# Performance work log

Measured on AMD Instinct MI355X. Metric: run time of the kernel, lower is better.

Reference implementation:

```python
import jax, jax.numpy as jnp
import numpy as np

B, S = 1, 1536
D_MODEL, NHEAD, HEAD_DIM = 1024, 16, 64
ROPE, NUM_SEQ = 32, 4
KVC, QC, D_FF = 256, 384, 4096
SPP = S // NUM_SEQ                      # seq per stock = 384
EPS_RMS = 1.1920929e-07                 # torch RMSNorm default eps = finfo(fp32).eps
ATTN_EPS = 1e-5
LAMBDA_INIT = 0.8 - 0.6 * float(np.exp(-0.3 * 0.0))  # depth 0 -> 0.2
SCALING = float(((HEAD_DIM + ROPE) // 2) ** -0.5)


def rmsnorm(x, w, eps=EPS_RMS):
    var = jnp.mean(jnp.square(x), axis=-1, keepdims=True)
    return x * jax.lax.rsqrt(var + eps) * w


def setup_inputs() -> dict:
    key = jax.random.key(0)
    ks = jax.random.split(key, 16)
    sd = 0.02
    inv_freq = 1.0 / (10000.0 ** (np.arange(0, ROPE // 4) / (ROPE // 4)))
    ang = np.arange(1, SPP)[:, None] * inv_freq[None, :]  # [SPP-1, ROPE//4]
    return {
        "x": jax.random.normal(ks[0], (B, S, D_MODEL), jnp.float32),
        "freqs_cos": jnp.asarray(np.cos(ang), jnp.float32),
        "freqs_sin": jnp.asarray(np.sin(ang), jnp.float32),
        "norm1_w": jnp.ones((D_MODEL,), jnp.float32),
        "norm2_w": jnp.ones((D_MODEL,), jnp.float32),
        "kv_down_w": jax.random.normal(ks[1], (KVC + ROPE, D_MODEL), jnp.float32) * sd,
        "q_down_w": jax.random.normal(ks[2], (QC, D_MODEL), jnp.float32) * sd,
        "kv_norm_w": jnp.ones((KVC,), jnp.float32),
        "q_norm_w": jnp.ones((QC,), jnp.float32),
        "kv_up_w": jax.random.normal(ks[3], (HEAD_DIM * NHEAD * 2, KVC), jnp.float32) * sd,
        "q_up_w": jax.random.normal(ks[4], ((HEAD_DIM + ROPE) * NHEAD, QC), jnp.float32) * sd,
        "lambda_q1": jax.random.normal(ks[5], (HEAD_DIM // 2,), jnp.float32) * 0.1,
        "lambda_k1": jax.random.normal(ks[6], (HEAD_DIM // 2,), jnp.float32) * 0.1,
        "lambda_q2": jax.random.normal(ks[7], (HEAD_DIM // 2,), jnp.float32) * 0.1,
        "lambda_k2": jax.random.normal(ks[8], (HEAD_DIM // 2,), jnp.float32) * 0.1,
        "attn_norm_w": jnp.ones((HEAD_DIM,), jnp.float32),
        "o_w": jax.random.normal(ks[9], (D_MODEL, NHEAD * HEAD_DIM), jnp.float32) * sd,
        "ff_in_w": jax.random.normal(ks[10], (D_FF * 2, D_MODEL), jnp.float32) * sd,
        "ff_out_w": jax.random.normal(ks[11], (D_MODEL, D_FF), jnp.float32) * sd,
    }


def reference(x, freqs_cos, freqs_sin, norm1_w, norm2_w, kv_down_w, q_down_w,
              kv_norm_w, q_norm_w, kv_up_w, q_up_w, lambda_q1, lambda_k1,
              lambda_q2, lambda_k2, attn_norm_w, o_w, ff_in_w, ff_out_w):
    b, s, _ = x.shape
    spp = s // NUM_SEQ
    H2, hd2 = 2 * NHEAD, HEAD_DIM // 2

    # block-tiled causal mask (1 = masked), matching mask.repeat(..., num_seq, num_seq)
    base = jnp.triu(jnp.ones((spp, spp), jnp.float32), 1)
    mask = jnp.tile(base, (NUM_SEQ, NUM_SEQ))  # [S, S]

    xin = rmsnorm(x, norm1_w)
    ckv = xin @ kv_down_w.T                                    # [B,S,KVC+ROPE]
    c_kv, k_rope = ckv[..., :KVC], ckv[..., KVC:]
    kv = (rmsnorm(c_kv, kv_norm_w) @ kv_up_w.T).reshape(b, s, NHEAD, 2 * HEAD_DIM)
    k, v = kv[..., :HEAD_DIM], kv[..., HEAD_DIM:]
    k = k.reshape(b, s, H2, hd2)
    qf = (rmsnorm(xin @ q_down_w.T, q_norm_w) @ q_up_w.T).reshape(b, s, NHEAD, HEAD_DIM + ROPE)
    q, q_rope = qf[..., :HEAD_DIM], qf[..., HEAD_DIM:]
    q = q.reshape(b, s, H2, hd2)
    k_rope = jnp.tile(k_rope[:, :, None, :], (1, 1, NHEAD, 1)).reshape(b, s, H2, ROPE // 2)
    q_rope = q_rope.reshape(b, s, H2, ROPE // 2)

    # rotary emb; position 0 of every ticker is left untouched (identity rotation)
    cos = jnp.concatenate([jnp.ones((1, ROPE // 4), freqs_cos.dtype), freqs_cos], 0)  # [spp, ROPE//4]
    sin = jnp.concatenate([jnp.zeros((1, ROPE // 4), freqs_sin.dtype), freqs_sin], 0)

    def rot(r):
        # S is laid out as (position, ticker) interleaved: s = p*NUM_SEQ + t
        r = r.reshape(b, spp, NUM_SEQ, H2, ROPE // 4, 2)
        c = cos[None, :, None, None, :]
        s_ = sin[None, :, None, None, :]
        r0, r1 = r[..., 0], r[..., 1]
        y = jnp.stack([r0 * c - r1 * s_, r0 * s_ + r1 * c], axis=-1)
        return y.reshape(b, s, H2, ROPE // 2)

    q = jnp.concatenate([q, rot(q_rope)], -1).transpose(0, 2, 1, 3)  # [B,2H,S,dk]
    k = jnp.concatenate([k, rot(k_rope)], -1).transpose(0, 2, 1, 3)
    v = v.transpose(0, 2, 1, 3)                                      # [B,H,S,hd]

    a = jnp.einsum('bhqd,bhkd->bhqk', q, k) * SCALING
    a = jnp.where(mask[None, None] == 1, -1e9, a)
    a = jax.nn.softmax(a, axis=-1)

    lam = jnp.exp(jnp.sum(lambda_k1 * lambda_q1)) - jnp.exp(jnp.sum(lambda_k2 * lambda_q2)) + LAMBDA_INIT
    a = a.reshape(b, NHEAD, 2, s, s)
    a1, a2 = a[:, :, 0], a[:, :, 1]
    g = jnp.mean(a1, axis=-2, keepdims=True)            # [B,H,1,S], broadcasts over queries
    a = a1 - lam * a2 + lam * g
    a = jnp.where(mask[None, None] == 1, 0.0, a)

    out = jnp.einsum('bhqk,bhkd->bhqd', a, v)           # [B,H,S,hd]
    out = rmsnorm(out.transpose(0, 2, 1, 3), attn_norm_w, eps=ATTN_EPS).transpose(0, 2, 1, 3)
    # faithful to source: raw reshape of [B,H,S,hd] -> [B,S,H*hd] (transposes cancel)
    out = out.reshape(b, s, NHEAD * HEAD_DIM)
    x = x + out @ o_w.T

    h = rmsnorm(x, norm2_w)
    uv = h @ ff_in_w.T
    u, vg = uv[..., :D_FF], uv[..., D_FF:]
    return x + (u * jax.nn.silu(vg)) @ ff_out_w.T
```

## Files before the change

### kernel.cpp

```cpp
#include <hip/hip_runtime.h>
#include <math.h>

#define S     1536
#define DM    1024
#define NH    16
#define H2N   32
#define HD    64
#define KVC   256
#define QC    384
#define DFF   4096
#define SPP   384
#define DQK   48
#define CKW   672
#define EPS_RMS  1.1920929e-07f
#define ATTN_EPS 1e-5f
#define SCALING  0.14433756729740643f

typedef float f32x4 __attribute__((ext_vector_type(4)));
typedef float f32x16 __attribute__((ext_vector_type(16)));
typedef short bf16x8 __attribute__((ext_vector_type(8)));

__device__ __forceinline__ short cvt_bf16(float f) {
  union { float f; unsigned u; } x; x.f = f;
  unsigned r = x.u + 0x7FFFu + ((x.u >> 16) & 1u);
  return (short)(r >> 16);
}
__device__ __forceinline__ unsigned pk2(float a, float b) {
  unsigned r;
  asm("v_cvt_pk_bf16_f32 %0, %1, %2" : "=v"(r) : "v"(a), "v"(b));
  return r;
}
__device__ __forceinline__ bf16x8 cvt8(float4 a, float4 b) {
  union { unsigned u[4]; bf16x8 v; } r;
  r.u[0] = pk2(a.x, a.y); r.u[1] = pk2(a.z, a.w);
  r.u[2] = pk2(b.x, b.y); r.u[3] = pk2(b.z, b.w);
  return r.v;
}
__device__ __forceinline__ int swz8(int flat, int nwg) {
  if (nwg & 7) return flat;
  return (flat & 7) * (nwg >> 3) + (flat >> 3);
}

__global__ __launch_bounds__(256) void cvt_w4(const float* __restrict__ s0, int n0,
    const float* __restrict__ s1, int n1, const float* __restrict__ s2, int n2,
    const float* __restrict__ s3, int n3, short* __restrict__ dst) {
  long base = (long)blockIdx.x * 2048 + (long)threadIdx.x * 8;
  const float* src; long off;
  if (base < n0) { src = s0; off = base; }
  else if (base < (long)n0 + n1) { src = s1; off = base - n0; }
  else if (base < (long)n0 + n1 + n2) { src = s2; off = base - n0 - n1; }
  else { src = s3; off = base - n0 - n1 - n2; }
  float4 a = *reinterpret_cast<const float4*>(src + off);
  float4 b = *reinterpret_cast<const float4*>(src + off + 4);
  *reinterpret_cast<bf16x8*>(dst + base) = cvt8(a, b);
}

__global__ __launch_bounds__(256) void rmsnorm_bf(const float* __restrict__ in,
    const float* __restrict__ w, short* __restrict__ out,
    int cols, int ldin, int ldout, float eps) {
  const int row = blockIdx.x;
  const float* xr = in + (size_t)row * ldin;
  short* yr = out + (size_t)row * ldout;
  const int tid = threadIdx.x;
  float ss = 0.f;
  for (int c = tid << 2; c < cols; c += 1024) {
    float4 v = *reinterpret_cast<const float4*>(xr + c);
    ss += v.x*v.x + v.y*v.y + v.z*v.z + v.w*v.w;
  }
#pragma unroll
  for (int mm = 1; mm < 64; mm <<= 1) ss += __shfl_xor(ss, mm, 64);
  __shared__ float red[4];
  if ((tid & 63) == 0) red[tid >> 6] = ss;
  __syncthreads();
  float tot = red[0] + red[1] + red[2] + red[3];
  float scale = rsqrtf(tot / (float)cols + eps);
  for (int c = tid << 2; c < cols; c += 1024) {
    float4 v = *reinterpret_cast<const float4*>(xr + c);
    float4 wv = *reinterpret_cast<const float4*>(w + c);
    uint2 p;
    p.x = pk2(v.x*scale*wv.x, v.y*scale*wv.y);
    p.y = pk2(v.z*scale*wv.z, v.w*scale*wv.w);
    *reinterpret_cast<uint2*>(yr + c) = p;
  }
}

__global__ __launch_bounds__(256) void rmsnorm2_bf(const float* __restrict__ comb,
    const float* __restrict__ w0, const float* __restrict__ w1,
    short* __restrict__ o0, short* __restrict__ o1, float eps) {
  const int row = blockIdx.x;
  const int seg = blockIdx.y;
  const float* xr = comb + (size_t)row * CKW + (seg ? 288 : 0);
  const float* w  = seg ? w1 : w0;
  short* yr = seg ? (o1 + (size_t)row * QC) : (o0 + (size_t)row * KVC);
  const int cols = seg ? QC : KVC;
  const int tid = threadIdx.x;
  float ss = 0.f;
  for (int c = tid << 2; c < cols; c += 1024) {
    float4 v = *reinterpret_cast<const float4*>(xr + c);
    ss += v.x*v.x + v.y*v.y + v.z*v.z + v.w*v.w;
  }
#pragma unroll
  for (int mm = 1; mm < 64; mm <<= 1) ss += __shfl_xor(ss, mm, 64);
  __shared__ float red[4];
  if ((tid & 63) == 0) red[tid >> 6] = ss;
  __syncthreads();
  float tot = red[0] + red[1] + red[2] + red[3];
  float scale = rsqrtf(tot / (float)cols + eps);
  for (int c = tid << 2; c < cols; c += 1024) {
    float4 v = *reinterpret_cast<const float4*>(xr + c);
    float4 wv = *reinterpret_cast<const float4*>(w + c);
    uint2 p;
    p.x = pk2(v.x*scale*wv.x, v.y*scale*wv.y);
    p.y = pk2(v.z*scale*wv.z, v.w*scale*wv.w);
    *reinterpret_cast<uint2*>(yr + c) = p;
  }
}

__global__ __launch_bounds__(256) void rmsnorm_sum_bf(const float* __restrict__ p0,
    const float* __restrict__ p1, const float* __restrict__ xres,
    const float* __restrict__ w, float* __restrict__ outw, short* __restrict__ yb,
    float eps) {
  const int row = blockIdx.x;
  const int c = threadIdx.x << 2;
  const size_t base = (size_t)row * DM + c;
  float4 a = *reinterpret_cast<const float4*>(p0 + base);
  float4 b = *reinterpret_cast<const float4*>(p1 + base);
  float4 xv = *reinterpret_cast<const float4*>(xres + base);
  float4 v = make_float4(a.x+b.x+xv.x, a.y+b.y+xv.y, a.z+b.z+xv.z, a.w+b.w+xv.w);
  *reinterpret_cast<float4*>(outw + base) = v;
  float ss = v.x*v.x + v.y*v.y + v.z*v.z + v.w*v.w;
#pragma unroll
  for (int mm = 1; mm < 64; mm <<= 1) ss += __shfl_xor(ss, mm, 64);
  __shared__ float red[4];
  if ((threadIdx.x & 63) == 0) red[threadIdx.x >> 6] = ss;
  __syncthreads();
  float tot = red[0] + red[1] + red[2] + red[3];
  float scale = rsqrtf(tot * (1.0f / (float)DM) + eps);
  float4 wv = *reinterpret_cast<const float4*>(w + c);
  uint2 p;
  p.x = pk2(v.x*scale*wv.x, v.y*scale*wv.y);
  p.y = pk2(v.z*scale*wv.z, v.w*scale*wv.w);
  *reinterpret_cast<uint2*>(yb + base) = p;
}

__global__ __launch_bounds__(256) void fadd2(float* __restrict__ out,
    const float* __restrict__ p0, const float* __restrict__ p1) {
  size_t i = ((size_t)blockIdx.x * 256 + threadIdx.x) << 2;
  float4 o = *reinterpret_cast<float4*>(out + i);
  float4 a = *reinterpret_cast<const float4*>(p0 + i);
  float4 b = *reinterpret_cast<const float4*>(p1 + i);
  o.x += a.x + b.x; o.y += a.y + b.y; o.z += a.z + b.z; o.w += a.w + b.w;
  *reinterpret_cast<float4*>(out + i) = o;
}

template<int ADD>
__global__ __launch_bounds__(256) void mgemm_nt(const short* __restrict__ A,
    const short* __restrict__ B, const float* __restrict__ src, float* __restrict__ C,
    int M, int N, int K, int lda, int ldb, int ldc) {
  __shared__ short As[64][72];
  __shared__ short Bs[64][72];
  const int nwg = gridDim.x * gridDim.y;
  const int sfl = swz8(blockIdx.y * gridDim.x + blockIdx.x, nwg);
  const int bxs = sfl % gridDim.x, bys = sfl / gridDim.x;
  const int bm = bys * 64, bn = bxs * 64;
  const int tid = threadIdx.x;
  const int w = tid >> 6, lane = tid & 63;
  const int wr = (w >> 1) << 5, wc = (w & 1) << 5;
  const int srow = tid >> 2, sk = (tid & 3) << 4;
  const int lrow = lane & 15, lk8 = (lane >> 4) << 3;
  const int arow = bm + srow, brow = bn + srow;
  const bool bvalid = brow < N;
  f32x4 acc[2][2];
#pragma unroll
  for (int i = 0; i < 2; ++i)
#pragma unroll
    for (int j = 0; j < 2; ++j) acc[i][j] = (f32x4){0.f, 0.f, 0.f, 0.f};

  bf16x8 rah0, rah1, rbh0, rbh1;
  {
    const short* ap = A + (size_t)arow * lda + sk;
    rah0 = *reinterpret_cast<const bf16x8*>(ap);
    rah1 = *reinterpret_cast<const bf16x8*>(ap + 8);
  }
  rbh0 = (bf16x8){0,0,0,0,0,0,0,0}; rbh1 = rbh0;
  if (bvalid) {
    const short* bp = B + (size_t)brow * ldb + sk;
    rbh0 = *reinterpret_cast<const bf16x8*>(bp);
    rbh1 = *reinterpret_cast<const bf16x8*>(bp + 8);
  }

  for (int k0 = 0; k0 < K; k0 += 64) {
    bf16x8 va0 = rah0, va1 = rah1, vb0 = rbh0, vb1 = rbh1;
    __syncthreads();
    *reinterpret_cast<bf16x8*>(&As[srow][sk])     = va0;
    *reinterpret_cast<bf16x8*>(&As[srow][sk + 8]) = va1;
    *reinterpret_cast<bf16x8*>(&Bs[srow][sk])     = vb0;
    *reinterpret_cast<bf16x8*>(&Bs[srow][sk + 8]) = vb1;
    __syncthreads();
// ... 41 lines not shown

__global__ __launch_bounds__(256) void mgemm_dual(const short* __restrict__ A0,
    const short* __restrict__ B0, float* __restrict__ C0,
    const short* __restrict__ A1, const short* __restrict__ B1, float* __restrict__ C1) {
  __shared__ short As[64][72];
  __shared__ short Bs[64][72];
  const int flat = blockIdx.x;
  const short *A, *B; float* C;
  int K, lda, ldb, ldc, bm, bn;
  if (flat < 768) {
    const int sfl = swz8(flat, 768);
    bm = (sfl / 32) * 64; bn = (sfl % 32) * 64;
    A = A0; B = B0; C = C0; K = KVC; lda = KVC; ldb = KVC; ldc = 2048;
  } else {
    const int sfl = swz8(flat - 768, 576);
    bm = (sfl / 24) * 64; bn = (sfl % 24) * 64;
    A = A1; B = B1; C = C1; K = QC; lda = QC; ldb = QC; ldc = 1536;
  }
  const int tid = threadIdx.x;
  const int w = tid >> 6, lane = tid & 63;
  const int wr = (w >> 1) << 5, wc = (w & 1) << 5;
  const int srow = tid >> 2, sk = (tid & 3) << 4;
  const int lrow = lane & 15, lk8 = (lane >> 4) << 3;
  const int arow = bm + srow, brow = bn + srow;
  f32x4 acc[2][2];
#pragma unroll
  for (int i = 0; i < 2; ++i)
#pragma unroll
    for (int j = 0; j < 2; ++j) acc[i][j] = (f32x4){0.f, 0.f, 0.f, 0.f};

  bf16x8 rah0, rah1, rbh0, rbh1;
  {
    const short* ap = A + (size_t)arow * lda + sk;
    rah0 = *reinterpret_cast<const bf16x8*>(ap);
    rah1 = *reinterpret_cast<const bf16x8*>(ap + 8);
    const short* bp = B + (size_t)brow * ldb + sk;
    rbh0 = *reinterpret_cast<const bf16x8*>(bp);
    rbh1 = *reinterpret_cast<const bf16x8*>(bp + 8);
  }
  for (int k0 = 0; k0 < K; k0 += 64) {
    bf16x8 va0 = rah0, va1 = rah1, vb0 = rbh0, vb1 = rbh1;
    __syncthreads();
    *reinterpret_cast<bf16x8*>(&As[srow][sk])     = va0;
    *reinterpret_cast<bf16x8*>(&As[srow][sk + 8]) = va1;
    *reinterpret_cast<bf16x8*>(&Bs[srow][sk])     = vb0;
    *reinterpret_cast<bf16x8*>(&Bs[srow][sk + 8]) = vb1;
    __syncthreads();
    const int kn = k0 + 64;
    if (kn < K) {
      const short* ap = A + (size_t)arow * lda + kn + sk;
      rah0 = *reinterpret_cast<const bf16x8*>(ap);
      rah1 = *reinterpret_cast<const bf16x8*>(ap + 8);
      const short* bp = B + (size_t)brow * ldb + kn + sk;
      rbh0 = *reinterpret_cast<const bf16x8*>(bp);
      rbh1 = *reinterpret_cast<const bf16x8*>(bp + 8);
    }
#pragma unroll
    for (int kk = 0; kk < 2; ++kk) {
      bf16x8 af0 = *reinterpret_cast<bf16x8*>(&As[wr + lrow][(kk << 5) + lk8]);
      bf16x8 af1 = *reinterpret_cast<bf16x8*>(&As[wr + 16 + lrow][(kk << 5) + lk8]);
      bf16x8 bf0 = *reinterpret_cast<bf16x8*>(&Bs[wc + lrow][(kk << 5) + lk8]);
      bf16x8 bf1 = *reinterpret_cast<bf16x8*>(&Bs[wc + 16 + lrow][(kk << 5) + lk8]);
      acc[0][0] = __builtin_amdgcn_mfma_f32_16x16x32_bf16(af0, bf0, acc[0][0], 0, 0, 0);
      acc[0][1] = __builtin_amdgcn_mfma_f32_16x16x32_bf16(af0, bf1, acc[0][1], 0, 0, 0);
      acc[1][0] = __builtin_amdgcn_mfma_f32_16x16x32_bf16(af1, bf0, acc[1][0], 0, 0, 0);
      acc[1][1] = __builtin_amdgcn_mfma_f32_16x16x32_bf16(af1, bf1, acc[1][1], 0, 0, 0);
    }
  }
  const int crow0 = bm + wr + ((lane >> 4) << 2);
  const int ccol0 = bn + wc + lrow;
#pragma unroll
  for (int mi = 0; mi < 2; ++mi)
#pragma unroll
    for (int ni = 0; ni < 2; ++ni) {
      int colc = ccol0 + (ni << 4);
#pragma unroll
      for (int r = 0; r < 4; ++r) {
        int rowc = crow0 + (mi << 4) + r;
        C[(size_t)rowc * ldc + colc] = acc[mi][ni][r];
      }
    }
}

__global__ __launch_bounds__(256) void mgemm_sk(const short* __restrict__ A,
    const short* __restrict__ B, float* __restrict__ P0, float* __restrict__ P1,
    int M, int N, int K2, int lda, int ldb, int ldc) {
  __shared__ short As[64][72];
  __shared__ short Bs[64][72];
  const int nwg = gridDim.x * gridDim.y;
  const int sfl = swz8(blockIdx.y * gridDim.x + blockIdx.x, nwg);
  const int bxs = sfl % gridDim.x, bys = sfl / gridDim.x;
  const int bm = bys * 64, bn = bxs * 64;
  const int koff = blockIdx.z * K2;
  float* C = blockIdx.z ? P1 : P0;
  const int tid = threadIdx.x;
  const int w = tid >> 6, lane = tid & 63;
  const int wr = (w >> 1) << 5, wc = (w & 1) << 5;
  const int srow = tid >> 2, sk = (tid & 3) << 4;
  const int lrow = lane & 15, lk8 = (lane >> 4) << 3;
  const int arow = bm + srow, brow = bn + srow;
  f32x4 acc[2][2];
#pragma unroll
  for (int i = 0; i < 2; ++i)
#pragma unroll
    for (int j = 0; j < 2; ++j) acc[i][j] = (f32x4){0.f, 0.f, 0.f, 0.f};

  bf16x8 rah0, rah1, rbh0, rbh1;
  {
    const short* ap = A + (size_t)arow * lda + koff + sk;
    rah0 = *reinterpret_cast<const bf16x8*>(ap);
    rah1 = *reinterpret_cast<const bf16x8*>(ap + 8);
    const short* bp = B + (size_t)brow * ldb + koff + sk;
    rbh0 = *reinterpret_cast<const bf16x8*>(bp);
    rbh1 = *reinterpret_cast<const bf16x8*>(bp + 8);
  }
  const int kend = koff + K2;
  for (int k0 = koff; k0 < kend; k0 += 64) {
    bf16x8 va0 = rah0, va1 = rah1, vb0 = rbh0, vb1 = rbh1;
    __syncthreads();
    *reinterpret_cast<bf16x8*>(&As[srow][sk])     = va0;
    *reinterpret_cast<bf16x8*>(&As[srow][sk + 8]) = va1;
    *reinterpret_cast<bf16x8*>(&Bs[srow][sk])     = vb0;
    *reinterpret_cast<bf16x8*>(&Bs[srow][sk + 8]) = vb1;
    __syncthreads();
    const int kn = k0 + 64;
    if (kn < kend) {
      const short* ap = A + (size_t)arow * lda + kn + sk;
      rah0 = *reinterpret_cast<const bf16x8*>(ap);
      rah1 = *reinterpret_cast<const bf16x8*>(ap + 8);
      const short* bp = B + (size_t)brow * ldb + kn + sk;
      rbh0 = *reinterpret_cast<const bf16x8*>(bp);
      rbh1 = *reinterpret_cast<const bf16x8*>(bp + 8);
    }
#pragma unroll
    for (int kk = 0; kk < 2; ++kk) {
      bf16x8 af0 = *reinterpret_cast<bf16x8*>(&As[wr + lrow][(kk << 5) + lk8]);
      bf16x8 af1 = *reinterpret_cast<bf16x8*>(&As[wr + 16 + lrow][(kk << 5) + lk8]);
      bf16x8 bf0 = *reinterpret_cast<bf16x8*>(&Bs[wc + lrow][(kk << 5) + lk8]);
      bf16x8 bf1 = *reinterpret_cast<bf16x8*>(&Bs[wc + 16 + lrow][(kk << 5) + lk8]);
      acc[0][0] = __builtin_amdgcn_mfma_f32_16x16x32_bf16(af0, bf0, acc[0][0], 0, 0, 0);
      acc[0][1] = __builtin_amdgcn_mfma_f32_16x16x32_bf16(af0, bf1, acc[0][1], 0, 0, 0);
      acc[1][0] = __builtin_amdgcn_mfma_f32_16x16x32_bf16(af1, bf0, acc[1][0], 0, 0, 0);
      acc[1][1] = __builtin_amdgcn_mfma_f32_16x16x32_bf16(af1, bf1, acc[1][1], 0, 0, 0);
    }
  }
  const int crow0 = bm + wr + ((lane >> 4) << 2);
  const int ccol0 = bn + wc + lrow;
#pragma unroll
  for (int mi = 0; mi < 2; ++mi)
#pragma unroll
    for (int ni = 0; ni < 2; ++ni) {
      int colc = ccol0 + (ni << 4);
#pragma unroll
      for (int r = 0; r < 4; ++r) {
        int rowc = crow0 + (mi << 4) + r;
        C[(size_t)rowc * ldc + colc] = acc[mi][ni][r];
      }
    }
}

__global__ __launch_bounds__(256) void mgemm_glu(const short* __restrict__ A,
    const short* __restrict__ Bw, short* __restrict__ C,
    int M, int N, int K, int lda, int ldb, int ldc) {
  __shared__ short As[128][72];
  __shared__ short Bu[64][72];
  __shared__ short Bv[64][72];
  const int nwg = gridDim.x * gridDim.y;
  const int sfl = swz8(blockIdx.y * gridDim.x + blockIdx.x, nwg);
  const int bxs = sfl % gridDim.x, bys = sfl / gridDim.x;
  const int bm = bys * 128, bn = bxs * 64;
  const int tid = threadIdx.x;
  const int w = tid >> 6, lane = tid & 63;
  const int wr = (w >> 1) << 6, wc = (w & 1) << 5;
  const int arow = bm + (tid >> 1), ac = (tid & 1) << 5;
  const int brow = bn + (tid >> 2), bc = (tid & 3) << 4;
  const int lrow = lane & 15, lk8 = (lane >> 4) << 3;
  f32x4 au[4][2], av[4][2];
#pragma unroll
  for (int i = 0; i < 4; ++i)
#pragma unroll
    for (int j = 0; j < 2; ++j) {
      au[i][j] = (f32x4){0.f, 0.f, 0.f, 0.f};
      av[i][j] = (f32x4){0.f, 0.f, 0.f, 0.f};
    }
  bf16x8 ra[4], ru[2], rv[2];
  {
    const short* ap = A + (size_t)arow * lda + ac;
    const short* up = Bw + (size_t)brow * ldb + bc;
    const short* vp = Bw + (size_t)(N + brow) * ldb + bc;
#pragma unroll
    for (int e = 0; e < 4; ++e) ra[e] = *reinterpret_cast<const bf16x8*>(ap + (e << 3));
    ru[0] = *reinterpret_cast<const bf16x8*>(up);
    ru[1] = *reinterpret_cast<const bf16x8*>(up + 8);
    rv[0] = *reinterpret_cast<const bf16x8*>(vp);
    rv[1] = *reinterpret_cast<const bf16x8*>(vp + 8);
  }
  for (int k0 = 0; k0 < K; k0 += 64) {
    __syncthreads();
#pragma unroll
    for (int e = 0; e < 4; ++e)
      *reinterpret_cast<bf16x8*>(&As[tid >> 1][ac + (e << 3)]) = ra[e];
    *reinterpret_cast<bf16x8*>(&Bu[tid >> 2][bc])     = ru[0];
    *reinterpret_cast<bf16x8*>(&Bu[tid >> 2][bc + 8]) = ru[1];
    *reinterpret_cast<bf16x8*>(&Bv[tid >> 2][bc])     = rv[0];
    *reinterpret_cast<bf16x8*>(&Bv[tid >> 2][bc + 8]) = rv[1];
    __syncthreads();
    const int kn = k0 + 64;
    if (kn < K) {
      const short* ap = A + (size_t)arow * lda + kn + ac;
      const short* up = Bw + (size_t)brow * ldb + kn + bc;
      const short* vp = Bw + (size_t)(N + brow) * ldb + kn + bc;
#pragma unroll
      for (int e = 0; e < 4; ++e) ra[e] = *reinterpret_cast<const bf16x8*>(ap + (e << 3));
      ru[0] = *reinterpret_cast<const bf16x8*>(up);
      ru[1] = *reinterpret_cast<const bf16x8*>(up + 8);
      rv[0] = *reinterpret_cast<const bf16x8*>(vp);
      rv[1] = *reinterpret_cast<const bf16x8*>(vp + 8);
    }
#pragma unroll
    for (int kk = 0; kk < 2; ++kk) {
      bf16x8 af[4], uf[2], vf[2];
#pragma unroll
      for (int i = 0; i < 4; ++i)
        af[i] = *reinterpret_cast<bf16x8*>(&As[wr + (i << 4) + lrow][(kk << 5) + lk8]);
#pragma unroll
      for (int j = 0; j < 2; ++j) {
        uf[j] = *reinterpret_cast<bf16x8*>(&Bu[wc + (j << 4) + lrow][(kk << 5) + lk8]);
        vf[j] = *reinterpret_cast<bf16x8*>(&Bv[wc + (j << 4) + lrow][(kk << 5) + lk8]);
      }
#pragma unroll
      for (int i = 0; i < 4; ++i)
#pragma unroll
        for (int j = 0; j < 2; ++j) {
          au[i][j] = __builtin_amdgcn_mfma_f32_16x16x32_bf16(af[i], uf[j], au[i][j], 0, 0, 0);
          av[i][j] = __builtin_amdgcn_mfma_f32_16x16x32_bf16(af[i], vf[j], av[i][j], 0, 0, 0);
        }
    }
  }
  const int crow0 = bm + wr + ((lane >> 4) << 2);
  const int ccol0 = bn + wc + lrow;
#pragma unroll
  for (int mi = 0; mi < 4; ++mi)
#pragma unroll
    for (int ni = 0; ni < 2; ++ni) {
      int colc = ccol0 + (ni << 4);
#pragma unroll
      for (int r = 0; r < 4; ++r) {
        int rowc = crow0 + (mi << 4) + r;
        float uu = au[mi][ni][r], vg = av[mi][ni][r];
        float sig = 1.0f / (1.0f + __expf(-vg));
        C[(size_t)rowc * ldc + colc] = cvt_bf16(uu * vg * sig);
      }
    }
}

__global__ __launch_bounds__(256) void prep_attn(const float* __restrict__ qf,
    const float* __restrict__ kvb, const float* __restrict__ ckv,
    const float* __restrict__ fc, const float* __restrict__ fs,
    short* __restrict__ Qb, short* __restrict__ Kb, short* __restrict__ Vt) {
  __shared__ short Ts[128][74];
  const int bx = blockIdx.x;
  if (bx < 192) {
    const int t = (bx % 6) * 256 + threadIdx.x;
    const int h2 = bx / 6;
    const int hh = h2 >> 1, par = h2 & 1;
    const float* qrow = qf + (size_t)t*1536 + hh*96;
    const float* krow = kvb + (size_t)t*2048 + hh*128;
    unsigned qu[24], ku[24];
#pragma unroll
    for (int xq = 0; xq < 8; ++xq) {
      float4 qv = *reinterpret_cast<const float4*>(qrow + par*32 + (xq<<2));
      float4 kv = *reinterpret_cast<const float4*>(krow + par*32 + (xq<<2));
      qu[xq*2]   = pk2(qv.x, qv.y); qu[xq*2+1] = pk2(qv.z, qv.w);
      ku[xq*2]   = pk2(kv.x, kv.y); ku[xq*2+1] = pk2(kv.z, kv.w);
    }
    int p = t >> 2;
    const float* qr = qrow + 64 + par*16;
    const float* kr = ckv + (size_t)t*CKW + 256 + par*16;
#pragma unroll
    for (int mq = 0; mq < 8; ++mq) {
      float c = 1.f, sn = 0.f;
      if (p > 0) { c = fc[(p-1)*8 + mq]; sn = fs[(p-1)*8 + mq]; }
      float q0 = qr[2*mq], q1 = qr[2*mq+1];
      qu[16 + mq] = pk2(q0*c - q1*sn, q0*sn + q1*c);
      float k0 = kr[2*mq], k1 = kr[2*mq+1];
      ku[16 + mq] = pk2(k0*c - k1*sn, k0*sn + k1*c);
    }
    unsigned* qo = (unsigned*)(Qb + ((size_t)h2*S + t)*DQK);
    unsigned* ko = (unsigned*)(Kb + ((size_t)h2*S + t)*DQK);
#pragma unroll
    for (int e = 0; e < 6; ++e) {
      *reinterpret_cast<uint4*>(qo + (e<<2)) = make_uint4(qu[e*4], qu[e*4+1], qu[e*4+2], qu[e*4+3]);
      *reinterpret_cast<uint4*>(ko + (e<<2)) = make_uint4(ku[e*4], ku[e*4+1], ku[e*4+2], ku[e*4+3]);
    }
  } else {
    const int f2 = bx - 192;
    const int hh = f2 % 16;
    const int t0 = (f2 / 16) << 7;
    const int tl = threadIdx.x >> 3, dp = (threadIdx.x & 7) << 3;
#pragma unroll
    for (int pass = 0; pass < 4; ++pass) {
      int t = t0 + (pass << 5) + tl;
      const float* vp = kvb + (size_t)t*2048 + hh*128 + 64 + dp;
      float4 a = *reinterpret_cast<const float4*>(vp);
      float4 b = *reinterpret_cast<const float4*>(vp + 4);
      *reinterpret_cast<bf16x8*>(&Ts[(pass << 5) + tl][dp]) = cvt8(a, b);
    }
    __syncthreads();
    for (int idx = threadIdx.x; idx < 1024; idx += 256) {
      int d = idx >> 4, tseg = (idx & 15) << 3;
      bf16x8 v;
#pragma unroll
      for (int e = 0; e < 8; ++e) v[e] = Ts[tseg + e][d];
      *reinterpret_cast<bf16x8*>(Vt + ((size_t)hh*HD + d)*S + t0 + tseg) = v;
    }
  }
}

__global__ __launch_bounds__(256) void flash_mfma(const short* __restrict__ Qb,
    const short* __restrict__ Kb, const short* __restrict__ Vg,
    float* __restrict__ Ob, float* __restrict__ rowm, float* __restrict__ rowl,
    float* __restrict__ Ob1a, float* __restrict__ Ob1b,
    float* __restrict__ rm1, float* __restrict__ rl1) {
  const int h2 = blockIdx.y;
  const int hh = h2 >> 1;
  const int z  = blockIdx.z;
  const int tid = threadIdx.x;
  const int w = tid >> 6, lane = tid & 63;
  const int ql = lane & 31, h = lane >> 5;
  const int cq = blockIdx.x / 3, k = blockIdx.x % 3;
  const int qi = k + 3*w;
  const int qbase = cq*SPP + (qi << 5);
  const int ri0w = qi << 5;

  __shared__ __align__(16) float Ot[4][32][36];

  bf16x8 qf0, qf1, qf2;
  {
    const short* qp = Qb + ((size_t)h2*S + qbase + ql)*DQK + (h << 3);
    qf0 = *reinterpret_cast<const bf16x8*>(qp);
    qf1 = *reinterpret_cast<const bf16x8*>(qp + 16);
    qf2 = *reinterpret_cast<const bf16x8*>(qp + 32);
  }
  const short* Kbase = Kb + (size_t)h2*S*DQK + (h << 3);
  const short* V0 = Vg + ((size_t)hh*HD + ql)*S + (h << 3);
  const short* V1 = Vg + ((size_t)hh*HD + 32 + ql)*S + (h << 3);

  float m = -1e30f, l = 0.f;
  f32x16 o0, o1;
#pragma unroll
  for (int r = 0; r < 16; ++r) { o0[r] = 0.f; o1[r] = 0.f; }

  for (int c = (z << 1); c < (z << 1) + 2; ++c) {
    for (int jr = 0; jr <= ri0w; jr += 32) {
      const int j0 = c*SPP + jr;
      const bool diag = (jr == ri0w);
      const short* kp = Kbase + (size_t)(j0 + ql)*DQK;
      bf16x8 kf0 = *reinterpret_cast<const bf16x8*>(kp);
      bf16x8 kf1 = *reinterpret_cast<const bf16x8*>(kp + 16);
      bf16x8 kf2 = *reinterpret_cast<const bf16x8*>(kp + 32);
      bf16x8 v00 = *reinterpret_cast<const bf16x8*>(V0 + j0);
      bf16x8 v01 = *reinterpret_cast<const bf16x8*>(V0 + j0 + 16);
      bf16x8 v10 = *reinterpret_cast<const bf16x8*>(V1 + j0);
      bf16x8 v11 = *reinterpret_cast<const bf16x8*>(V1 + j0 + 16);

      f32x16 st;
#pragma unroll
      for (int r = 0; r < 16; ++r) st[r] = 0.f;
      st = __builtin_amdgcn_mfma_f32_32x32x16_bf16(kf0, qf0, st, 0, 0, 0);
      st = __builtin_amdgcn_mfma_f32_32x32x16_bf16(kf1, qf1, st, 0, 0, 0);
      st = __builtin_amdgcn_mfma_f32_32x32x16_bf16(kf2, qf2, st, 0, 0, 0);

      if (diag) {
#pragma unroll
        for (int r = 0; r < 16; ++r) {
          int kl = (r & 3) + ((r >> 2) << 3) + (h << 2);
          st[r] = (kl <= ql) ? st[r] * SCALING : -1e30f;
        }
      } else {
#pragma unroll
        for (int r = 0; r < 16; ++r) st[r] *= SCALING;
      }

      float tm = st[0];
#pragma unroll
      for (int r = 1; r < 16; ++r) tm = fmaxf(tm, st[r]);
      tm = fmaxf(tm, __shfl_xor(tm, 32));
      if (__any(tm > m + 8.0f)) {
        float mnew = fmaxf(m, tm);
        float sc = __expf(m - mnew);
        m = mnew;
        l *= sc;
#pragma unroll
        for (int r = 0; r < 16; ++r) { o0[r] *= sc; o1[r] *= sc; }
      }
      float ps = 0.f;
#pragma unroll
      for (int r = 0; r < 16; ++r) { float p = __expf(st[r] - m); st[r] = p; ps += p; }
      ps += __shfl_xor(ps, 32);
      l += ps;

      unsigned A0 = pk2(st[0],  st[1]),  B0 = pk2(st[2],  st[3]);
      unsigned C0 = pk2(st[4],  st[5]),  D0 = pk2(st[6],  st[7]);
      unsigned A1 = pk2(st[8],  st[9]),  B1 = pk2(st[10], st[11]);
      unsigned C1 = pk2(st[12], st[13]), D1 = pk2(st[14], st[15]);
      unsigned xA0 = (unsigned)__shfl_xor((int)A0, 32), xB0 = (unsigned)__shfl_xor((int)B0, 32);
      unsigned xC0 = (unsigned)__shfl_xor((int)C0, 32), xD0 = (unsigned)__shfl_xor((int)D0, 32);
      unsigned xA1 = (unsigned)__shfl_xor((int)A1, 32), xB1 = (unsigned)__shfl_xor((int)B1, 32);
      unsigned xC1 = (unsigned)__shfl_xor((int)C1, 32), xD1 = (unsigned)__shfl_xor((int)D1, 32);
      union { unsigned u[4]; bf16x8 v; } P0, P1;
      P0.u[0] = h ? xC0 : A0;  P0.u[1] = h ? xD0 : B0;
      P0.u[2] = h ? C0 : xA0;  P0.u[3] = h ? D0 : xB0;
      P1.u[0] = h ? xC1 : A1;  P1.u[1] = h ? xD1 : B1;
      P1.u[2] = h ? C1 : xA1;  P1.u[3] = h ? D1 : xB1;

      o0 = __builtin_amdgcn_mfma_f32_32x32x16_bf16(v00, P0.v, o0, 0, 0, 0);
      o0 = __builtin_amdgcn_mfma_f32_32x32x16_bf16(v01, P1.v, o0, 0, 0, 0);
      o1 = __builtin_amdgcn_mfma_f32_32x32x16_bf16(v10, P0.v, o1, 0, 0, 0);
      o1 = __builtin_amdgcn_mfma_f32_32x32x16_bf16(v11, P1.v, o1, 0, 0, 0);
    }
  }

  float* ot = &Ot[w][0][0];
  float* orow;
  if (z == 0) orow = Ob + ((size_t)h2*S + qbase)*HD;
  else orow = (h2 < 16) ? Ob1a + ((size_t)h2*S + qbase)*HD
                        : Ob1b + ((size_t)(h2 - 16)*S + qbase)*HD;
#pragma unroll
  for (int r = 0; r < 16; ++r) {
    int dl = (r & 3) + ((r >> 2) << 3) + (h << 2);
    ot[ql*36 + dl] = o0[r];
  }
#pragma unroll
  for (int it = 0; it < 4; ++it) {
    int idx = lane + (it << 6);
    int row = idx >> 3, c4 = (idx & 7) << 2;
    float4 v = *reinterpret_cast<float4*>(&ot[row*36 + c4]);
    *reinterpret_cast<float4*>(&orow[(size_t)row*HD + c4]) = v;
  }
#pragma unroll
  for (int r = 0; r < 16; ++r) {
    int dl = (r & 3) + ((r >> 2) << 3) + (h << 2);
    ot[ql*36 + dl] = o1[r];
  }
#pragma unroll
  for (int it = 0; it < 4; ++it) {
    int idx = lane + (it << 6);
    int row = idx >> 3, c4 = (idx & 7) << 2;
    float4 v = *reinterpret_cast<float4*>(&ot[row*36 + c4]);
    *reinterpret_cast<float4*>(&orow[(size_t)row*HD + 32 + c4]) = v;
  }
  if (lane < 32) {
    if (z == 0) { rowm[h2*S + qbase + lane] = m; rowl[h2*S + qbase + lane] = l; }
    else        { rm1[h2*S + qbase + lane] = m;  rl1[h2*S + qbase + lane] = l; }
  }
}

__global__ __launch_bounds__(256) void merge_ml(float* __restrict__ rowm,
    float* __restrict__ rowl, float* __restrict__ rm1, float* __restrict__ rl1,
    const float* __restrict__ lq1, const float* __restrict__ lk1,
    const float* __restrict__ lq2, const float* __restrict__ lk2,
    float* __restrict__ lamp) {
  const int gid = blockIdx.x * 256 + threadIdx.x;
  float m0 = rowm[gid], l0 = rowl[gid], m1 = rm1[gid], l1 = rl1[gid];
  float m = fmaxf(m0, m1);
  float w0 = __expf(m0 - m), w1 = __expf(m1 - m);
  float L = l0*w0 + l1*w1;
  float linv = 1.0f / L;
  rowm[gid] = m; rowl[gid] = L;
  rm1[gid] = w0 * linv; rl1[gid] = w1 * linv;
  if (blockIdx.x == 0 && threadIdx.x < 32) {
    int t = threadIdx.x;
    float a = lq1[t]*lk1[t];
    float b = lq2[t]*lk2[t];
#pragma unroll
    for (int mm = 1; mm < 32; mm <<= 1) { a += __shfl_xor(a, mm, 32); b += __shfl_xor(b, mm, 32); }
    if (t == 0) lamp[0] = expf(a) - expf(b) + 0.2f;
  }
}

__global__ __launch_bounds__(256) void colsum_mfma(const short* __restrict__ Qb,
    const short* __restrict__ Kb, const float* __restrict__ rowm,
    const float* __restrict__ rowl, float* __restrict__ gcol) {
  const int jt = blockIdx.x;
  const int hh = blockIdx.y, h2 = hh << 1;
  const int cK = jt / 12, jr32 = jt % 12;
  const int jr = jr32 << 5;
  const int j0 = cK*SPP + jr;
  const int tid = threadIdx.x;
  const int w = tid >> 6, lane = tid & 63;
  const int ql = lane & 31, h = lane >> 5;

  bf16x8 kf0, kf1, kf2;
  {
    const short* kp = Kb + ((size_t)h2*S + j0 + ql)*DQK + (h << 3);
    kf0 = *reinterpret_cast<const bf16x8*>(kp);
    kf1 = *reinterpret_cast<const bf16x8*>(kp + 16);
    kf2 = *reinterpret_cast<const bf16x8*>(kp + 32);
  }
  const int nt = 12 - jr32;
  const int T = nt << 2;
  float gs[16];
#pragma unroll
  for (int r = 0; r < 16; ++r) gs[r] = 0.f;

  for (int tt = w; tt < T; tt += 4) {
    int cq = tt / nt, qrem = tt - cq*nt;
    int qi = jr32 + qrem;
    int i0 = cq*SPP + (qi << 5);
    const bool diag = (qrem == 0);
    const short* qp = Qb + ((size_t)h2*S + i0 + ql)*DQK + (h << 3);
    bf16x8 qf0 = *reinterpret_cast<const bf16x8*>(qp);
    bf16x8 qf1 = *reinterpret_cast<const bf16x8*>(qp + 16);
    bf16x8 qf2 = *reinterpret_cast<const bf16x8*>(qp + 32);
    f32x16 st;
#pragma unroll
    for (int r = 0; r < 16; ++r) st[r] = 0.f;
    st = __builtin_amdgcn_mfma_f32_32x32x16_bf16(kf0, qf0, st, 0, 0, 0);
    st = __builtin_amdgcn_mfma_f32_32x32x16_bf16(kf1, qf1, st, 0, 0, 0);
    st = __builtin_amdgcn_mfma_f32_32x32x16_bf16(kf2, qf2, st, 0, 0, 0);
    float Mq = rowm[h2*S + i0 + ql];
    float Lq = 1.0f / rowl[h2*S + i0 + ql];
    if (diag) {
#pragma unroll
      for (int r = 0; r < 16; ++r) {
        int kl = (r & 3) + ((r >> 2) << 3) + (h << 2);
        if (kl <= ql) gs[r] += __expf(st[r]*SCALING - Mq) * Lq;
      }
    } else {
#pragma unroll
      for (int r = 0; r < 16; ++r) gs[r] += __expf(st[r]*SCALING - Mq) * Lq;
    }
  }
  __shared__ float gw[4][32];
#pragma unroll
  for (int r = 0; r < 16; ++r) {
    float v = gs[r];
#pragma unroll
    for (int mm = 1; mm < 32; mm <<= 1) v += __shfl_xor(v, mm, 32);
    if (ql == 0) gw[w][(r & 3) + ((r >> 2) << 3) + (h << 2)] = v;
  }
  __syncthreads();
  if (tid < 32) {
    float s = gw[0][tid] + gw[1][tid] + gw[2][tid] + gw[3][tid];
    gcol[hh*S + j0 + tid] = s * (1.0f / (float)S);
  }
}

__global__ __launch_bounds__(256) void build_wpre(const float* __restrict__ gcol,
    const float* __restrict__ kvb, float* __restrict__ Wpre) {
  const int hh = blockIdx.x >> 2;
  const int dq = (blockIdx.x & 3) << 4;
  __shared__ float Wt[SPP][16];
  const int tid = threadIdx.x;
  for (int idx = tid; idx < SPP*16; idx += 256) {
    int r = idx >> 4, dd = idx & 15;
    float val = 0.f;
#pragma unroll
    for (int b2 = 0; b2 < 4; ++b2) {
      int j = b2*SPP + r;
      val = fmaf(gcol[hh*S + j], kvb[(size_t)j*2048 + hh*128 + 64 + dq + dd], val);
    }
    Wt[r][dd] = val;
  }
  __syncthreads();
  if (tid < 16) {
    float run = 0.f;
    for (int r = 0; r < SPP; ++r) { run += Wt[r][tid]; Wt[r][tid] = run; }
  }
  __syncthreads();
  for (int idx = tid; idx < SPP*16; idx += 256) {
    int r = idx >> 4, dd = idx & 15;
    Wpre[((size_t)hh*SPP + r)*HD + dq + dd] = Wt[r][dd];
  }
}

__global__ __launch_bounds__(256) void combine_rms(const float* __restrict__ Ob,
    const float* __restrict__ Ob1a, const float* __restrict__ Ob1b,
    const float* __restrict__ a0v, const float* __restrict__ a1v,
    const float* __restrict__ Wpre, const float* __restrict__ lamp,
    const float* __restrict__ anw, short* __restrict__ attno) {
  const int t = blockIdx.x * 4 + (threadIdx.x >> 6);
  const int h = blockIdx.y;
  const int d = threadIdx.x & 63;
  const float lam = lamp[0];
  const int g1 = (2*h)*S + t, g2 = (2*h+1)*S + t;
  const float* p1 = (h < 8) ? (Ob1a + (size_t)g1*HD) : (Ob1b + ((size_t)g1 - (size_t)16*S)*HD);
  const float* p2 = (h < 8) ? (Ob1a + (size_t)g2*HD) : (Ob1b + ((size_t)g2 - (size_t)16*S)*HD);
  float o1 = Ob[(size_t)g1*HD + d] * a0v[g1] + p1[d] * a1v[g1];
  float o2 = Ob[(size_t)g2*HD + d] * a0v[g2] + p2[d] * a1v[g2];
  const float w3 = Wpre[((size_t)h*SPP + (t % SPP))*HD + d];
  float val = o1 - lam*o2 + lam*w3;
  float ss = val*val;
#pragma unroll
  for (int mm = 1; mm < 64; mm <<= 1) ss += __shfl_xor(ss, mm, 64);
  float scale = rsqrtf(ss * (1.0f/HD) + ATTN_EPS) * anw[d];
  int tn = h*96 + (t >> 4);
  int cn = ((t & 15) << 6) + d;
  attno[(size_t)tn*DM + cn] = cvt_bf16(val * scale);
}

extern "C" void kernel_launch(void* const* d_in, const int* in_sizes, int n_in,
                              void* d_out, int out_size, void* d_ws, size_t ws_size,
                              hipStream_t stream) {
  (void)in_sizes; (void)n_in; (void)out_size;
  const float* x    = (const float*)d_in[0];
  const float* fc   = (const float*)d_in[1];
  const float* fs   = (const float*)d_in[2];
  const float* n1w  = (const float*)d_in[3];
  const float* n2w  = (const float*)d_in[4];
  const float* kvdw = (const float*)d_in[5];
  const float* qdw  = (const float*)d_in[6];
  const float* kvnw = (const float*)d_in[7];
  const float* qnw  = (const float*)d_in[8];
  const float* kvuw = (const float*)d_in[9];
  const float* quw  = (const float*)d_in[10];
  const float* lq1  = (const float*)d_in[11];
  const float* lk1  = (const float*)d_in[12];
  const float* lq2  = (const float*)d_in[13];
  const float* lk2  = (const float*)d_in[14];
  const float* anw  = (const float*)d_in[15];
  const float* ow   = (const float*)d_in[16];
  const float* ffiw = (const float*)d_in[17];
  const float* ffow = (const float*)d_in[18];
  float* out = (float*)d_out;
  float* ws  = (float*)d_ws;

  float* xin   = ws;
  float* ckv   = xin   + (size_t)S*DM;
  float* qmid  = ckv   + (size_t)S*288;
  float* kvb   = qmid  + (size_t)S*QC;
  float* qf    = kvb   + (size_t)S*2048;
  float* Qb    = qf    + (size_t)S*1536;
  float* Kb    = Qb    + (size_t)H2N*S*DQK;
  float* Obuf  = Kb    + (size_t)H2N*S*DQK;
  float* rowm  = Obuf  + (size_t)H2N*S*HD;
  float* rowl  = rowm  + (size_t)H2N*S;
  float* gcol  = rowl  + (size_t)H2N*S;
  float* Wpre  = gcol  + (size_t)NH*S;
  float* attno = Wpre  + (size_t)NH*SPP*HD;
  float* lamp  = attno + (size_t)S*DM;
  short* fbufs = (short*)kvb;
  float* Ob1a = xin;
  float* Ob1b = qf;
  float* rm1  = qf + (size_t)16*S*HD;
  float* rl1  = rm1 + (size_t)H2N*S;
  short* Qb_bf = (short*)Qb;
  short* Kb_bf = (short*)Kb;
  short* Vt_bf = (short*)Qb + 2359296;
  short* xin_bf  = (short*)xin;
  short* ckv_bf  = (short*)Obuf;
  short* qmid_bf = ckv_bf + (size_t)S*KVC;
  short* h_bf    = (short*)ckv;
  short* attno_bf = (short*)attno;
  short* kvdw_bf = (short*)attno;
  short* qdw_bf  = kvdw_bf + 294912;
  short* kvuw_bf = qdw_bf  + 393216;
  short* quw_bf  = kvuw_bf + 524288;
  short* ffiw_bf = (short*)Qb;
  short* ow_bf   = ffiw_bf + 8388608;
  short* ffow_bf = (short*)Obuf;
  float* psum0 = xin;
  float* psum1 = qf;
  if (ws_size < (size_t)18063376 * sizeof(float)) return;

  cvt_w4<<<880, 256, 0, stream>>>(kvdw, 294912, qdw, 393216, kvuw, 524288, quw, 589824, kvdw_bf);
  rmsnorm_bf<<<S, 256, 0, stream>>>(x, n1w, xin_bf, DM, DM, DM, EPS_RMS);
  { dim3 g(11, 24); mgemm_nt<0><<<g, 256, 0, stream>>>(xin_bf, kvdw_bf, nullptr, ckv, S, CKW, DM, DM, DM, CKW); }
  { dim3 g(S, 2);   rmsnorm2_bf<<<g, 256, 0, stream>>>(ckv, kvnw, qnw, ckv_bf, qmid_bf, EPS_RMS); }
  mgemm_dual<<<1344, 256, 0, stream>>>(ckv_bf, kvuw_bf, kvb, qmid_bf, quw_bf, qf);
  prep_attn<<<384, 256, 0, stream>>>(qf, kvb, ckv, fc, fs, Qb_bf, Kb_bf, Vt_bf);
  { dim3 g(12, 32, 2); flash_mfma<<<g, 256, 0, stream>>>(Qb_bf, Kb_bf, Vt_bf, Obuf, rowm, rowl,
                                                         Ob1a, Ob1b, rm1, rl1); }
  merge_ml<<<(H2N*S)/256, 256, 0, stream>>>(rowm, rowl, rm1, rl1, lq1, lk1, lq2, lk2, lamp);
  { dim3 g(48, 16); colsum_mfma<<<g, 256, 0, stream>>>(Qb_bf, Kb_bf, rowm, rowl, gcol); }
  cvt_w4<<<4608, 256, 0, stream>>>(ffiw, 8388608, ow, 1048576, nullptr, 0, nullptr, 0, ffiw_bf);
  build_wpre<<<64, 256, 0, stream>>>(gcol, kvb, Wpre);
  { dim3 g(S/4, 16); combine_rms<<<g, 256, 0, stream>>>(Obuf, Ob1a, Ob1b, rm1, rl1,
                                                        Wpre, lamp, anw, attno_bf); }
  cvt_w4<<<2048, 256, 0, stream>>>(ffow, 4194304, nullptr, 0, nullptr, 0, nullptr, 0, ffow_bf);
  { dim3 g(16, 24, 2); mgemm_sk<<<g, 256, 0, stream>>>(attno_bf, ow_bf, psum0, psum1, S, DM, 512, DM, DM, DM); }
  rmsnorm_sum_bf<<<S, 256, 0, stream>>>(psum0, psum1, x, n2w, out, h_bf, EPS_RMS);
  { dim3 g(64, 12); mgemm_glu<<<g, 256, 0, stream>>>(h_bf, ffiw_bf, fbufs, S, DFF, DM, DM, DM, DFF); }
  { dim3 g(16, 24, 2); mgemm_sk<<<g, 256, 0, stream>>>(fbufs, ffow_bf, psum0, psum1, S, DM, 2048, DFF, DFF, DM); }
  fadd2<<<1536, 256, 0, stream>>>(out, psum0, psum1);
}
```

Measured before the change: 210.8 us.

## Fuse weight conversions into neighboring kernels and raise MFMA wave priority

Each standalone fp32-to-bf16 weight conversion launch is merged into an adjacent kernel as extra blocks: one with the first RMSNorm, one with build_wpre, one with the O-projection split-K GEMM. This cuts launch count and lets the bandwidth-bound conversion overlap with compute-bound work. It also wraps the MFMA sequences in the GLU GEMM, flash attention and colsum kernels with s_setprio raises. The merged kernels have mixed block types, which can unbalance scheduling and raise shared-memory and register needs for the conversion blocks.

```diff
diff --git a/kernel.cpp b/kernel.cpp
--- a/kernel.cpp
+++ b/kernel.cpp
@@ -41,26 +41,8 @@
   return (flat & 7) * (nwg >> 3) + (flat >> 3);
 }
 
-__global__ __launch_bounds__(256) void cvt_w4(const float* __restrict__ s0, int n0,
-    const float* __restrict__ s1, int n1, const float* __restrict__ s2, int n2,
-    const float* __restrict__ s3, int n3, short* __restrict__ dst) {
-  long base = (long)blockIdx.x * 2048 + (long)threadIdx.x * 8;
-  const float* src; long off;
-  if (base < n0) { src = s0; off = base; }
-  else if (base < (long)n0 + n1) { src = s1; off = base - n0; }
-  else if (base < (long)n0 + n1 + n2) { src = s2; off = base - n0 - n1; }
-  else { src = s3; off = base - n0 - n1 - n2; }
-  float4 a = *reinterpret_cast<const float4*>(src + off);
-  float4 b = *reinterpret_cast<const float4*>(src + off + 4);
-  *reinterpret_cast<bf16x8*>(dst + base) = cvt8(a, b);
-}
-
-__global__ __launch_bounds__(256) void rmsnorm_bf(const float* __restrict__ in,
-    const float* __restrict__ w, short* __restrict__ out,
-    int cols, int ldin, int ldout, float eps) {
-  const int row = blockIdx.x;
-  const float* xr = in + (size_t)row * ldin;
-  short* yr = out + (size_t)row * ldout;
+__device__ __forceinline__ void rms_body(const float* xr, const float* w,
+    short* yr, int cols, float eps) {
   const int tid = threadIdx.x;
   float ss = 0.f;
   for (int c = tid << 2; c < cols; c += 1024) {
@@ -84,36 +66,36 @@
   }
 }
 
+__global__ __launch_bounds__(256) void rms1_cvt(const float* __restrict__ x,
+    const float* __restrict__ n1w, short* __restrict__ xin_bf,
+    const float* __restrict__ s0, int n0, const float* __restrict__ s1, int n1,
+    const float* __restrict__ s2, int n2, const float* __restrict__ s3,
+    short* __restrict__ dst) {
+  const int bx = blockIdx.x;
+  if (bx < S) {
+    rms_body(x + (size_t)bx * DM, n1w, xin_bf + (size_t)bx * DM, DM, EPS_RMS);
+  } else {
+    long base = (long)(bx - S) * 2048 + (long)threadIdx.x * 8;
+    const float* src; long off;
+    if (base < n0) { src = s0; off = base; }
+    else if (base < (long)n0 + n1) { src = s1; off = base - n0; }
+    else if (base < (long)n0 + n1 + n2) { src = s2; off = base - n0 - n1; }
+    else { src = s3; off = base - n0 - n1 - n2; }
+    float4 a = *reinterpret_cast<const float4*>(src + off);
+    float4 b = *reinterpret_cast<const float4*>(src + off + 4);
+    *reinterpret_cast<bf16x8*>(dst + base) = cvt8(a, b);
+  }
+}
+
 __global__ __launch_bounds__(256) void rmsnorm2_bf(const float* __restrict__ comb,
     const float* __restrict__ w0, const float* __restrict__ w1,
     short* __restrict__ o0, short* __restrict__ o1, float eps) {
   const int row = blockIdx.x;
   const int seg = blockIdx.y;
   const float* xr = comb + (size_t)row * CKW + (seg ? 288 : 0);
-  const float* w  = seg ? w1 : w0;
-  short* yr = seg ? (o1 + (size_t)row * QC) : (o0 + (size_t)row * KVC);
-  const int cols = seg ? QC : KVC;
-  const int tid = threadIdx.x;
-  float ss = 0.f;
-  for (int c = tid << 2; c < cols; c += 1024) {
-    float4 v = *reinterpret_cast<const float4*>(xr + c);
-    ss += v.x*v.x + v.y*v.y + v.z*v.z + v.w*v.w;
-  }
-#pragma unroll
-  for (int mm = 1; mm < 64; mm <<= 1) ss += __shfl_xor(ss, mm, 64);
-  __shared__ float red[4];
-  if ((tid & 63) == 0) red[tid >> 6] = ss;
-  __syncthreads();
-  float tot = red[0] + red[1] + red[2] + red[3];
-  float scale = rsqrtf(tot / (float)cols + eps);
-  for (int c = tid << 2; c < cols; c += 1024) {
-    float4 v = *reinterpret_cast<const float4*>(xr + c);
-    float4 wv = *reinterpret_cast<const float4*>(w + c);
-    uint2 p;
-    p.x = pk2(v.x*scale*wv.x, v.y*scale*wv.y);
-    p.y = pk2(v.z*scale*wv.z, v.w*scale*wv.w);
-    *reinterpret_cast<uint2*>(yr + c) = p;
-  }
+  rms_body(xr, seg ? w1 : w0,
+           seg ? (o1 + (size_t)row * QC) : (o0 + (size_t)row * KVC),
+           seg ? QC : KVC, eps);
 }
 
 __global__ __launch_bounds__(256) void rmsnorm_sum_bf(const float* __restrict__ p0,
@@ -321,17 +303,11 @@
     }
 }
 
-__global__ __launch_bounds__(256) void mgemm_sk(const short* __restrict__ A,
-    const short* __restrict__ B, float* __restrict__ P0, float* __restrict__ P1,
-    int M, int N, int K2, int lda, int ldb, int ldc) {
+__device__ __forceinline__ void sk_body(const short* __restrict__ A,
+    const short* __restrict__ B, float* __restrict__ C,
+    int bm, int bn, int koff, int K2, int lda, int ldb, int ldc) {
   __shared__ short As[64][72];
   __shared__ short Bs[64][72];
-  const int nwg = gridDim.x * gridDim.y;
-  const int sfl = swz8(blockIdx.y * gridDim.x + blockIdx.x, nwg);
-  const int bxs = sfl % gridDim.x, bys = sfl / gridDim.x;
-  const int bm = bys * 64, bn = bxs * 64;
-  const int koff = blockIdx.z * K2;
-  float* C = blockIdx.z ? P1 : P0;
   const int tid = threadIdx.x;
   const int w = tid >> 6, lane = tid & 63;
   const int wr = (w >> 1) << 5, wc = (w & 1) << 5;
@@ -398,6 +374,32 @@
     }
 }
 
+__global__ __launch_bounds__(256) void mgemm_sk(const short* __restrict__ A,
+    const short* __restrict__ B, float* __restrict__ P0, float* __restrict__ P1,
+    int M, int N, int K2, int lda, int ldb, int ldc) {
+  const int nwg = gridDim.x * gridDim.y;
+  const int sfl = swz8(blockIdx.y * gridDim.x + blockIdx.x, nwg);
+  sk_body(A, B, blockIdx.z ? P1 : P0, (sfl / gridDim.x) * 64,
+          (sfl % gridDim.x) * 64, blockIdx.z * K2, K2, lda, ldb, ldc);
+}
+
+__global__ __launch_bounds__(256) void oproj_cvt(const short* __restrict__ A,
+    const short* __restrict__ B, float* __restrict__ P0, float* __restrict__ P1,
+    const float* __restrict__ ffow, short* __restrict__ ffow_bf) {
+  const int bx = blockIdx.x;
+  if (bx < 768) {
+    const int z = bx >= 384;
+    const int sfl = swz8(bx - (z ? 384 : 0), 384);
+    sk_body(A, B, z ? P1 : P0, (sfl / 16) * 64, (sfl % 16) * 64,
+            z * 512, 512, DM, DM, DM);
+  } else {
+    long base = (long)(bx - 768) * 2048 + (long)threadIdx.x * 8;
+    float4 a = *reinterpret_cast<const float4*>(ffow + base);
+    float4 b = *reinterpret_cast<const float4*>(ffow + base + 4);
+    *reinterpret_cast<bf16x8*>(ffow_bf + base) = cvt8(a, b);
+  }
+}
+
 __global__ __launch_bounds__(256) void mgemm_glu(const short* __restrict__ A,
     const short* __restrict__ Bw, short* __restrict__ C,
     int M, int N, int K, int lda, int ldb, int ldc) {
@@ -467,6 +469,7 @@
         uf[j] = *reinterpret_cast<bf16x8*>(&Bu[wc + (j << 4) + lrow][(kk << 5) + lk8]);
         vf[j] = *reinterpret_cast<bf16x8*>(&Bv[wc + (j << 4) + lrow][(kk << 5) + lk8]);
       }
+      __builtin_amdgcn_s_setprio(1);
 #pragma unroll
       for (int i = 0; i < 4; ++i)
 #pragma unroll
@@ -474,6 +477,7 @@
           au[i][j] = __builtin_amdgcn_mfma_f32_16x16x32_bf16(af[i], uf[j], au[i][j], 0, 0, 0);
           av[i][j] = __builtin_amdgcn_mfma_f32_16x16x32_bf16(af[i], vf[j], av[i][j], 0, 0, 0);
         }
+      __builtin_amdgcn_s_setprio(0);
     }
   }
   const int crow0 = bm + wr + ((lane >> 4) << 2);
@@ -606,9 +610,11 @@
       f32x16 st;
 #pragma unroll
       for (int r = 0; r < 16; ++r) st[r] = 0.f;
+      __builtin_amdgcn_s_setprio(1);
       st = __builtin_amdgcn_mfma_f32_32x32x16_bf16(kf0, qf0, st, 0, 0, 0);
       st = __builtin_amdgcn_mfma_f32_32x32x16_bf16(kf1, qf1, st, 0, 0, 0);
       st = __builtin_amdgcn_mfma_f32_32x32x16_bf16(kf2, qf2, st, 0, 0, 0);
+      __builtin_amdgcn_s_setprio(0);
 
       if (diag) {
 #pragma unroll
@@ -653,10 +659,12 @@
       P1.u[0] = h ? xC1 : A1;  P1.u[1] = h ? xD1 : B1;
       P1.u[2] = h ? C1 : xA1;  P1.u[3] = h ? D1 : xB1;
 
+      __builtin_amdgcn_s_setprio(1);
       o0 = __builtin_amdgcn_mfma_f32_32x32x16_bf16(v00, P0.v, o0, 0, 0, 0);
       o0 = __builtin_amdgcn_mfma_f32_32x32x16_bf16(v01, P1.v, o0, 0, 0, 0);
       o1 = __builtin_amdgcn_mfma_f32_32x32x16_bf16(v10, P0.v, o1, 0, 0, 0);
       o1 = __builtin_amdgcn_mfma_f32_32x32x16_bf16(v11, P1.v, o1, 0, 0, 0);
+      __builtin_amdgcn_s_setprio(0);
     }
   }
 
@@ -755,9 +763,11 @@
     f32x16 st;
 #pragma unroll
     for (int r = 0; r < 16; ++r) st[r] = 0.f;
+    __builtin_amdgcn_s_setprio(1);
     st = __builtin_amdgcn_mfma_f32_32x32x16_bf16(kf0, qf0, st, 0, 0, 0);
     st = __builtin_amdgcn_mfma_f32_32x32x16_bf16(kf1, qf1, st, 0, 0, 0);
     st = __builtin_amdgcn_mfma_f32_32x32x16_bf16(kf2, qf2, st, 0, 0, 0);
+    __builtin_amdgcn_s_setprio(0);
     float Mq = rowm[h2*S + i0 + ql];
     float Lq = 1.0f / rowl[h2*S + i0 + ql];
     if (diag) {
@@ -786,10 +796,23 @@
   }
 }
 
-__global__ __launch_bounds__(256) void build_wpre(const float* __restrict__ gcol,
-    const float* __restrict__ kvb, float* __restrict__ Wpre) {
-  const int hh = blockIdx.x >> 2;
-  const int dq = (blockIdx.x & 3) << 4;
+__global__ __launch_bounds__(256) void wpre_cvt(const float* __restrict__ gcol,
+    const float* __restrict__ kvb, float* __restrict__ Wpre,
+    const float* __restrict__ ffiw, const float* __restrict__ ow,
+    short* __restrict__ ffiw_bf) {
+  const int bx = blockIdx.x;
+  if (bx >= 64) {
+    long base = (long)(bx - 64) * 2048 + (long)threadIdx.x * 8;
+    const float* src; long off;
+    if (base < 8388608L) { src = ffiw; off = base; }
+    else { src = ow; off = base - 8388608L; }
+    float4 a = *reinterpret_cast<const float4*>(src + off);
+    float4 b = *reinterpret_cast<const float4*>(src + off + 4);
+    *reinterpret_cast<bf16x8*>(ffiw_bf + base) = cvt8(a, b);
+    return;
+  }
+  const int hh = bx >> 2;
+  const int dq = (bx & 3) << 4;
   __shared__ float Wt[SPP][16];
   const int tid = threadIdx.x;
   for (int idx = tid; idx < SPP*16; idx += 256) {
@@ -903,8 +926,8 @@
   float* psum1 = qf;
   if (ws_size < (size_t)18063376 * sizeof(float)) return;
 
-  cvt_w4<<<880, 256, 0, stream>>>(kvdw, 294912, qdw, 393216, kvuw, 524288, quw, 589824, kvdw_bf);
-  rmsnorm_bf<<<S, 256, 0, stream>>>(x, n1w, xin_bf, DM, DM, DM, EPS_RMS);
+  rms1_cvt<<<S + 880, 256, 0, stream>>>(x, n1w, xin_bf,
+      kvdw, 294912, qdw, 393216, kvuw, 524288, quw, kvdw_bf);
   { dim3 g(11, 24); mgemm_nt<0><<<g, 256, 0, stream>>>(xin_bf, kvdw_bf, nullptr, ckv, S, CKW, DM, DM, DM, CKW); }
   { dim3 g(S, 2);   rmsnorm2_bf<<<g, 256, 0, stream>>>(ckv, kvnw, qnw, ckv_bf, qmid_bf, EPS_RMS); }
   mgemm_dual<<<1344, 256, 0, stream>>>(ckv_bf, kvuw_bf, kvb, qmid_bf, quw_bf, qf);
@@ -913,12 +936,10 @@
                                                          Ob1a, Ob1b, rm1, rl1); }
   merge_ml<<<(H2N*S)/256, 256, 0, stream>>>(rowm, rowl, rm1, rl1, lq1, lk1, lq2, lk2, lamp);
   { dim3 g(48, 16); colsum_mfma<<<g, 256, 0, stream>>>(Qb_bf, Kb_bf, rowm, rowl, gcol); }
-  cvt_w4<<<4608, 256, 0, stream>>>(ffiw, 8388608, ow, 1048576, nullptr, 0, nullptr, 0, ffiw_bf);
-  build_wpre<<<64, 256, 0, stream>>>(gcol, kvb, Wpre);
+  wpre_cvt<<<64 + 4608, 256, 0, stream>>>(gcol, kvb, Wpre, ffiw, ow, ffiw_bf);
   { dim3 g(S/4, 16); combine_rms<<<g, 256, 0, stream>>>(Obuf, Ob1a, Ob1b, rm1, rl1,
                                                         Wpre, lamp, anw, attno_bf); }
-  cvt_w4<<<2048, 256, 0, stream>>>(ffow, 4194304, nullptr, 0, nullptr, 0, nullptr, 0, ffow_bf);
-  { dim3 g(16, 24, 2); mgemm_sk<<<g, 256, 0, stream>>>(attno_bf, ow_bf, psum0, psum1, S, DM, 512, DM, DM, DM); }
+  oproj_cvt<<<768 + 2048, 256, 0, stream>>>(attno_bf, ow_bf, psum0, psum1, ffow, ffow_bf);
   rmsnorm_sum_bf<<<S, 256, 0, stream>>>(psum0, psum1, x, n2w, out, h_bf, EPS_RMS);
   { dim3 g(64, 12); mgemm_glu<<<g, 256, 0, stream>>>(h_bf, ffiw_bf, fbufs, S, DFF, DM, DM, DM, DFF); }
   { dim3 g(16, 24, 2); mgemm_sk<<<g, 256, 0, stream>>>(fbufs, ffow_bf, psum0, psum1, S, DM, 2048, DFF, DFF, DM); }
```

After: 202.6 us. -3.9%, faster.
